# Kernel tuning notes

Hardware: AMD Instinct MI355X
Metric: run time of the kernel (lower is better)

Reference implementation:

```python
import jax, jax.numpy as jnp
import numpy as np

T = 2048          # num tokens (prefill)
H = 4096          # hidden_size
NH = 32           # num query heads
NKV = 8           # num kv heads (GQA)
HD = H // NH      # head_dim = 128
BASE = 1000000.0  # rope_theta
NEG = -1e30


def _rope(x, positions):
    # NeoX-style rotary embedding (vLLM default). x: [T, nh, HD]
    half = HD // 2
    inv_freq = 1.0 / (BASE ** (jnp.arange(half, dtype=jnp.float32) / half))
    freqs = positions.astype(jnp.float32)[:, None] * inv_freq  # [T, half]
    cos = jnp.concatenate([jnp.cos(freqs), jnp.cos(freqs)], -1)[:, None, :]
    sin = jnp.concatenate([jnp.sin(freqs), jnp.sin(freqs)], -1)[:, None, :]
    rot = jnp.concatenate([-x[..., half:], x[..., :half]], -1)
    return x * cos + rot * sin


def setup_inputs() -> dict:
    key = jax.random.key(0)
    k1, k2, k3 = jax.random.split(key, 3)
    hidden_states = jax.random.normal(k1, (T, H), jnp.float32)
    wqkv = jax.random.normal(k2, (H, (NH + 2 * NKV) * HD), jnp.float32) * 0.02
    wo = jax.random.normal(k3, (NH * HD, H), jnp.float32) * 0.02
    positions = jnp.arange(T, dtype=jnp.int32)
    return {"positions": positions, "hidden_states": hidden_states,
            "wqkv": wqkv, "wo": wo}


def reference(positions, hidden_states, wqkv, wo):
    # fused QKV projection
    qkv = hidden_states @ wqkv                      # [T, (NH+2*NKV)*HD]
    q, k, v = jnp.split(qkv, [NH * HD, NH * HD + NKV * HD], axis=-1)
    q = q.reshape(T, NH, HD)
    k = k.reshape(T, NKV, HD)
    v = v.reshape(T, NKV, HD)
    # inline RoPE on q, k
    q = _rope(q, positions)
    k = _rope(k, positions)
    # GQA: expand kv heads to query heads
    rep = NH // NKV
    k = jnp.repeat(k, rep, axis=1)                  # [T, NH, HD]
    v = jnp.repeat(v, rep, axis=1)
    # causal scaled dot-product attention (prefill path of PagedAttention)
    scores = jnp.einsum('qhd,khd->hqk', q, k) * (HD ** -0.5)  # [NH, T, T]
    causal = positions[:, None] >= positions[None, :]          # [T, T]
    scores = jnp.where(causal[None, :, :], scores, NEG)
    probs = jax.nn.softmax(scores, axis=-1)
    attn = jnp.einsum('hqk,khd->qhd', probs, v).reshape(T, NH * HD)
    return attn @ wo
```

## Files before the change

kernel.cpp:

```cpp
#include <hip/hip_runtime.h>
#include <hip/hip_bf16.h>

typedef __attribute__((ext_vector_type(8))) short bf16x8;
typedef __attribute__((ext_vector_type(4))) float f32x4;
typedef unsigned short u16;

#define T_TOK 2048
#define HID 4096
#define NH 32
#define NKV 8
#define HD 128
#define QKVN 6144
#define KOFF 4096
#define VOFF 5120
#define ATTN_SCALE 0.08838834764831845f

static __device__ __forceinline__ float bf2f(u16 x) {
    union { float f; unsigned u; } v; v.u = ((unsigned)x) << 16; return v.f;
}
static __device__ __forceinline__ u16 f2bf(float f) {
    union { float f; unsigned u; } v; v.f = f;
    unsigned u = v.u;
    unsigned r = (u + 0x7fff + ((u >> 16) & 1)) >> 16;
    return (u16)r;
}

static __device__ __forceinline__ void gload16(const u16* g, u16* l) {
    __builtin_amdgcn_global_load_lds((const __attribute__((address_space(1))) void*)g,
                                     (__attribute__((address_space(3))) void*)l, 16, 0, 0);
}

#define VMC(n) asm volatile("s_waitcnt vmcnt(%0)" :: "i"(n) : "memory")
#define LGKM0() asm volatile("s_waitcnt lgkmcnt(0)" ::: "memory")
#define BAR() __builtin_amdgcn_s_barrier()
#define SCHB() __builtin_amdgcn_sched_barrier(0)

__global__ __launch_bounds__(256) void convk(const float* __restrict__ in, u16* __restrict__ out) {
    int i = blockIdx.x * 256 + threadIdx.x;
    float4 v = ((const float4*)in)[i];
    ushort4 o;
    o.x = f2bf(v.x); o.y = f2bf(v.y); o.z = f2bf(v.z); o.w = f2bf(v.w);
    ((ushort4*)out)[i] = o;
}

__global__ __launch_bounds__(256) void transpk(const float* __restrict__ in, u16* __restrict__ out,
                                               int R, int C) {
    __shared__ float tile[64][65];
    int c0 = blockIdx.x * 64, r0 = blockIdx.y * 64;
    int tid = threadIdx.x;
#pragma unroll
    for (int it = 0; it < 4; ++it) {
        int ci = it * 256 + tid;
        int r = ci >> 4, c4 = (ci & 15) * 4;
        float4 v = *(const float4*)&in[(size_t)(r0 + r) * C + c0 + c4];
        tile[r][c4 + 0] = v.x; tile[r][c4 + 1] = v.y; tile[r][c4 + 2] = v.z; tile[r][c4 + 3] = v.w;
    }
    __syncthreads();
#pragma unroll
    for (int it = 0; it < 4; ++it) {
        int ci = it * 256 + tid;
        int c = ci >> 4, rq = (ci & 15) * 4;
        ushort4 o;
        o.x = f2bf(tile[rq + 0][c]); o.y = f2bf(tile[rq + 1][c]);
        o.z = f2bf(tile[rq + 2][c]); o.w = f2bf(tile[rq + 3][c]);
        *(ushort4*)&out[(size_t)(c0 + c) * R + r0 + rq] = o;
    }
}

template <int BN, int OUTF32>
__global__ __launch_bounds__(512) void gemm4p(const u16* __restrict__ A, const u16* __restrict__ Bt,
                                              void* __restrict__ Cout, int M, int N, int K) {
    constexpr int NF = BN / 64;
    constexpr int LB = BN / 128;
    constexpr int DBUF = (128 + BN) * 64;
    constexpr int BHALF = (BN / 2) * 64;
    __shared__ __attribute__((aligned(16))) u16 lds[2 * DBUF];

    int bid = blockIdx.x;
    int m0 = (bid & 15) * 128, n0 = (bid >> 4) * BN;
    int tid = threadIdx.x, lane = tid & 63, wid = tid >> 6;
    int wm = wid >> 2, wn = wid & 3;
    int l15 = lane & 15, g4 = lane >> 4;
    int sw = l15 & 7;
    int srow = tid >> 3;
    int sslot8 = (((tid & 7) ^ ((tid >> 3) & 7))) * 8;
    int brow0 = (wn & 1) * (BN / 4);
    int NK = K / 64;

    auto STAGE_A = [&](int kt, int h) {
        gload16(&A[(size_t)(m0 + h * 64 + srow) * K + kt * 64 + sslot8],
                &lds[(kt & 1) * DBUF + h * 4096 + wid * 512]);
    };
    auto STAGE_B = [&](int kt, int bh) {
#pragma unroll
        for (int it = 0; it < LB; ++it)
            gload16(&Bt[(size_t)(n0 + bh * (BN / 2) + it * 64 + srow) * K + kt * 64 + sslot8],
                    &lds[(kt & 1) * DBUF + 8192 + bh * BHALF + it * 4096 + wid * 512]);
    };

    f32x4 acc[4][NF];
#pragma unroll
    for (int i = 0; i < 4; ++i)
#pragma unroll
        for (int j = 0; j < NF; ++j) acc[i][j] = (f32x4){0.f, 0.f, 0.f, 0.f};

    STAGE_A(0, 0); STAGE_A(0, 1); STAGE_B(0, 0); STAGE_B(0, 1);
    STAGE_A(1, 0); STAGE_A(1, 1); STAGE_B(1, 0); STAGE_B(1, 1);
    VMC(2 + 2 * LB);
    BAR(); SCHB();

    for (int g = 0; g < NK; ++g) {
        const u16* dd = &lds[(g & 1) * DBUF];
        const u16* aw = dd + wm * 4096;
        const u16* bw = dd + 8192 + (wn >> 1) * BHALF;
        bool mid = (g > 0) && (g + 1 < NK);
        bf16x8 bfr[NF], af0, af1;

#pragma unroll
        for (int nf = 0; nf < NF; ++nf)
            bfr[nf] = *(const bf16x8*)&bw[(brow0 + nf * 16 + l15) * 64 + ((g4 ^ sw) * 8)];
        af0 = *(const bf16x8*)&aw[(0 * 16 + l15) * 64 + ((g4 ^ sw) * 8)];
        af1 = *(const bf16x8*)&aw[(1 * 16 + l15) * 64 + ((g4 ^ sw) * 8)];
        if (mid) STAGE_A(g + 1, 0);
        BAR(); LGKM0();
        __builtin_amdgcn_s_setprio(1);
#pragma unroll
        for (int nf = 0; nf < NF; ++nf) {
            acc[0][nf] = __builtin_amdgcn_mfma_f32_16x16x32_bf16(af0, bfr[nf], acc[0][nf], 0, 0, 0);
            acc[1][nf] = __builtin_amdgcn_mfma_f32_16x16x32_bf16(af1, bfr[nf], acc[1][nf], 0, 0, 0);
        }
        __builtin_amdgcn_s_setprio(0);
        BAR();

        af0 = *(const bf16x8*)&aw[(2 * 16 + l15) * 64 + ((g4 ^ sw) * 8)];
        af1 = *(const bf16x8*)&aw[(3 * 16 + l15) * 64 + ((g4 ^ sw) * 8)];
        if (mid) STAGE_B(g + 1, 1);
        BAR(); LGKM0();
        __builtin_amdgcn_s_setprio(1);
#pragma unroll
        for (int nf = 0; nf < NF; ++nf) {
            acc[2][nf] = __builtin_amdgcn_mfma_f32_16x16x32_bf16(af0, bfr[nf], acc[2][nf], 0, 0, 0);
            acc[3][nf] = __builtin_amdgcn_mfma_f32_16x16x32_bf16(af1, bfr[nf], acc[3][nf], 0, 0, 0);
        }
        __builtin_amdgcn_s_setprio(0);
        BAR();

#pragma unroll
        for (int nf = 0; nf < NF; ++nf)
            bfr[nf] = *(const bf16x8*)&bw[(brow0 + nf * 16 + l15) * 64 + (((4 + g4) ^ sw) * 8)];
        af0 = *(const bf16x8*)&aw[(0 * 16 + l15) * 64 + (((4 + g4) ^ sw) * 8)];
        af1 = *(const bf16x8*)&aw[(1 * 16 + l15) * 64 + (((4 + g4) ^ sw) * 8)];
        if (mid) STAGE_A(g + 1, 1);
        BAR(); LGKM0();
        __builtin_amdgcn_s_setprio(1);
#pragma unroll
        for (int nf = 0; nf < NF; ++nf) {
            acc[0][nf] = __builtin_amdgcn_mfma_f32_16x16x32_bf16(af0, bfr[nf], acc[0][nf], 0, 0, 0);
            acc[1][nf] = __builtin_amdgcn_mfma_f32_16x16x32_bf16(af1, bfr[nf], acc[1][nf], 0, 0, 0);
        }
        __builtin_amdgcn_s_setprio(0);
        BAR();

        af0 = *(const bf16x8*)&aw[(2 * 16 + l15) * 64 + (((4 + g4) ^ sw) * 8)];
        af1 = *(const bf16x8*)&aw[(3 * 16 + l15) * 64 + (((4 + g4) ^ sw) * 8)];
        if (g + 2 < NK) STAGE_B(g + 2, 0);
        BAR(); LGKM0();
        __builtin_amdgcn_s_setprio(1);
#pragma unroll
        for (int nf = 0; nf < NF; ++nf) {
            acc[2][nf] = __builtin_amdgcn_mfma_f32_16x16x32_bf16(af0, bfr[nf], acc[2][nf], 0, 0, 0);
            acc[3][nf] = __builtin_amdgcn_mfma_f32_16x16x32_bf16(af1, bfr[nf], acc[3][nf], 0, 0, 0);
        }
        __builtin_amdgcn_s_setprio(0);
        if (g <= NK - 3)      VMC(LB);
        else if (g == NK - 2) VMC(0);
        BAR(); SCHB();
    }

#pragma unroll
    for (int mf = 0; mf < 4; ++mf)
#pragma unroll
        for (int nf = 0; nf < NF; ++nf)
#pragma unroll
            for (int i = 0; i < 4; ++i) {
                int row = m0 + wm * 64 + mf * 16 + g4 * 4 + i;
                int col = n0 + wn * (BN / 4) + nf * 16 + l15;
                float v = acc[mf][nf][i];
                if (OUTF32) ((float*)Cout)[(size_t)row * N + col] = v;
                else        ((u16*)Cout)[(size_t)row * N + col] = f2bf(v);
            }
}

__global__ __launch_bounds__(256) void ropek(u16* __restrict__ qkvb, const int* __restrict__ positions) {
    __shared__ float cs_[64], sn_[64];
    int t = blockIdx.x;
    float pos = (float)positions[t];
    if (threadIdx.x < 64) {
        int d = threadIdx.x;
        float inv = exp2f(-(float)d * (19.931568569324174f / 64.0f));
        float fr = pos * inv;
        cs_[d] = cosf(fr);
        sn_[d] = sinf(fr);
    }
    __syncthreads();
#pragma unroll
    for (int it = 0; it < 10; ++it) {
        int ci = it * 256 + threadIdx.x;
        int hh = ci >> 6, d = ci & 63;
        int base = (hh < NH) ? hh * HD : KOFF + (hh - NH) * HD;
        size_t off = (size_t)t * QKVN + base + d;
        float x1 = bf2f(qkvb[off]);
        float x2 = bf2f(qkvb[off + 64]);
        float s = sn_[d], c = cs_[d];
        float y1 = x1 * c - x2 * s;
        float y2 = x2 * c + x1 * s;
        if (hh < NH) { y1 *= ATTN_SCALE; y2 *= ATTN_SCALE; }
        qkvb[off]      = f2bf(y1);
        qkvb[off + 64] = f2bf(y2);
    }
}

__global__ __launch_bounds__(256) void vtranspk(const u16* __restrict__ qkvb, u16* __restrict__ vT) {
    __shared__ __attribute__((aligned(16))) u16 tile[64][136];
    int kvh = blockIdx.x, t0 = blockIdx.y * 64;
    int tid = threadIdx.x;
#pragma unroll
    for (int it = 0; it < 4; ++it) {
        int ci = it * 256 + tid;
        int r = ci >> 4, c8 = (ci & 15) * 8;
        *(bf16x8*)&tile[r][c8] = *(const bf16x8*)&qkvb[(size_t)(t0 + r) * QKVN + VOFF + kvh * HD + c8];
    }
    __syncthreads();
#pragma unroll
    for (int it = 0; it < 4; ++it) {
        int ci = it * 256 + tid;
        int d = ci >> 3, tc = (ci & 7) * 8;
        union { bf16x8 v; u16 u[8]; } o;
#pragma unroll
        for (int e = 0; e < 8; ++e) o.u[e] = tile[tc + e][d];
        *(bf16x8*)&vT[((size_t)kvh * HD + d) * T_TOK + t0 + tc] = o.v;
    }
}

__global__ __launch_bounds__(512) void attnk(const u16* __restrict__ qkvb, const u16* __restrict__ vT,
                                             u16* __restrict__ attnb) {
    __shared__ __attribute__((aligned(16))) u16 kt_[64 * 136];
    __shared__ __attribute__((aligned(16))) u16 vt_[128 * 72];
    __shared__ __attribute__((aligned(16))) u16 pl_[8 * 16 * 72];
    int h = blockIdx.x, qt = 15 - blockIdx.y;
    int kvh = h >> 2;
    int q0 = qt * 128;
    int tid = threadIdx.x, lane = tid & 63, wid = tid >> 6;
    int l15 = lane & 15, g = lane >> 4;

    const u16* kbase = qkvb + KOFF + (size_t)kvh * HD;
    const u16* vbase = vT + (size_t)kvh * HD * T_TOK;

    bf16x8 qf[4];
    int qrow = q0 + wid * 16 + l15;
#pragma unroll
    for (int ks = 0; ks < 4; ++ks)
        qf[ks] = *(const bf16x8*)&qkvb[(size_t)qrow * QKVN + h * HD + ks * 32 + g * 8];

    f32x4 o[8];
#pragma unroll
    for (int df = 0; df < 8; ++df) o[df] = (f32x4){0.f, 0.f, 0.f, 0.f};
    float m_run[4], l_run[4];
#pragma unroll
    for (int i = 0; i < 4; ++i) { m_run[i] = -3.0e38f; l_run[i] = 0.f; }

    int NT = 2 * qt + 2;

    bf16x8 kreg[2], vreg[2];
#pragma unroll
    for (int it = 0; it < 2; ++it) {
        int gi = it * 512 + tid;
        kreg[it] = *(const bf16x8*)&kbase[(size_t)(gi >> 4) * QKVN + (gi & 15) * 8];
        vreg[it] = *(const bf16x8*)&vbase[(size_t)(gi >> 3) * T_TOK + (gi & 7) * 8];
    }
#pragma unroll
    for (int it = 0; it < 2; ++it) {
        int gi = it * 512 + tid;
        *(bf16x8*)&kt_[(gi >> 4) * 136 + (gi & 15) * 8] = kreg[it];
        *(bf16x8*)&vt_[(gi >> 3) * 72 + (gi & 7) * 8] = vreg[it];
    }
#pragma unroll
    for (int it = 0; it < 2; ++it) {
        int gi = it * 512 + tid;
        kreg[it] = *(const bf16x8*)&kbase[(size_t)(64 + (gi >> 4)) * QKVN + (gi & 15) * 8];
        vreg[it] = *(const bf16x8*)&vbase[(size_t)(gi >> 3) * T_TOK + 64 + (gi & 7) * 8];
    }
    __syncthreads();

    for (int kt2 = 0; kt2 < NT; ++kt2) {
        int kvb = kt2 * 64;
        bool active = (kvb <= q0 + wid * 16 + 15);
        bool diag   = (kvb + 63 > q0 + wid * 16);

        if (active) {
            f32x4 s[4];
#pragma unroll
            for (int nf = 0; nf < 4; ++nf) s[nf] = (f32x4){0.f, 0.f, 0.f, 0.f};
            __builtin_amdgcn_s_setprio(1);
#pragma unroll
            for (int ks = 0; ks < 4; ++ks) {
#pragma unroll
                for (int nf = 0; nf < 4; ++nf) {
                    bf16x8 bfr = *(const bf16x8*)&kt_[(nf * 16 + l15) * 136 + ks * 32 + g * 8];
                    s[nf] = __builtin_amdgcn_mfma_f32_16x16x32_bf16(qf[ks], bfr, s[nf], 0, 0, 0);
                }
            }
            __builtin_amdgcn_s_setprio(0);

            float mrow[4];
#pragma unroll
            for (int i = 0; i < 4; ++i) {
                int qr = q0 + wid * 16 + g * 4 + i;
                float mx = -3.0e38f;
#pragma unroll
                for (int nf = 0; nf < 4; ++nf) {
                    float v = s[nf][i];
                    if (diag) {
                        int kvc = kvb + nf * 16 + l15;
                        v = (kvc <= qr) ? v : -1.0e30f;
                        s[nf][i] = v;
                    }
                    mx = fmaxf(mx, v);
                }
                mrow[i] = mx;
            }
#pragma unroll
            for (int dd = 1; dd < 16; dd <<= 1)
#pragma unroll
                for (int i = 0; i < 4; ++i) mrow[i] = fmaxf(mrow[i], __shfl_xor(mrow[i], dd));

            int ok = 1;
#pragma unroll
            for (int i = 0; i < 4; ++i) ok &= (mrow[i] <= m_run[i] + 8.0f) ? 1 : 0;
            if (!__all(ok)) {
                float alpha[4];
#pragma unroll
                for (int i = 0; i < 4; ++i) {
                    float mnew = fmaxf(m_run[i], mrow[i]);
                    alpha[i] = __expf(m_run[i] - mnew);
                    m_run[i] = mnew;
                    l_run[i] *= alpha[i];
                }
#pragma unroll
                for (int df = 0; df < 8; ++df)
#pragma unroll
                    for (int i = 0; i < 4; ++i) o[df][i] *= alpha[i];
            }

            float rsum[4] = {0.f, 0.f, 0.f, 0.f};
#pragma unroll
            for (int nf = 0; nf < 4; ++nf)
#pragma unroll
                for (int i = 0; i < 4; ++i) {
                    float p = __expf(s[nf][i] - m_run[i]);
                    rsum[i] += p;
                    pl_[wid * 1152 + (g * 4 + i) * 72 + nf * 16 + l15] = f2bf(p);
                }
#pragma unroll
            for (int dd = 1; dd < 16; dd <<= 1)
#pragma unroll
                for (int i = 0; i < 4; ++i) rsum[i] += __shfl_xor(rsum[i], dd);
#pragma unroll
            for (int i = 0; i < 4; ++i) l_run[i] += rsum[i];

            __builtin_amdgcn_s_setprio(1);
#pragma unroll
            for (int ks2 = 0; ks2 < 2; ++ks2) {
                bf16x8 af = *(const bf16x8*)&pl_[wid * 1152 + l15 * 72 + ks2 * 32 + g * 8];
#pragma unroll
                for (int df = 0; df < 8; ++df) {
                    bf16x8 bfr = *(const bf16x8*)&vt_[(df * 16 + l15) * 72 + ks2 * 32 + g * 8];
                    o[df] = __builtin_amdgcn_mfma_f32_16x16x32_bf16(af, bfr, o[df], 0, 0, 0);
                }
            }
            __builtin_amdgcn_s_setprio(0);
        }

        if (kt2 < NT - 1) {
            __syncthreads();
#pragma unroll
            for (int it = 0; it < 2; ++it) {
                int gi = it * 512 + tid;
                *(bf16x8*)&kt_[(gi >> 4) * 136 + (gi & 15) * 8] = kreg[it];
                *(bf16x8*)&vt_[(gi >> 3) * 72 + (gi & 7) * 8] = vreg[it];
            }
            int ktl = (kt2 + 2 < NT) ? kt2 + 2 : NT - 1;
#pragma unroll
            for (int it = 0; it < 2; ++it) {
                int gi = it * 512 + tid;
                kreg[it] = *(const bf16x8*)&kbase[(size_t)(ktl * 64 + (gi >> 4)) * QKVN + (gi & 15) * 8];
                vreg[it] = *(const bf16x8*)&vbase[(size_t)(gi >> 3) * T_TOK + ktl * 64 + (gi & 7) * 8];
            }
            __syncthreads();
        }
    }

#pragma unroll
    for (int df = 0; df < 8; ++df)
#pragma unroll
        for (int i = 0; i < 4; ++i) {
            int qr = q0 + wid * 16 + g * 4 + i;
            int col = h * HD + df * 16 + l15;
            attnb[(size_t)qr * (NH * HD) + col] = f2bf(o[df][i] / l_run[i]);
        }
}

extern "C" void kernel_launch(void* const* d_in, const int* in_sizes, int n_in,
                              void* d_out, int out_size, void* d_ws, size_t ws_size,
                              hipStream_t stream) {
    const int*   positions = (const int*)d_in[0];
    const float* hs        = (const float*)d_in[1];
    const float* wqkv      = (const float*)d_in[2];
    const float* wo        = (const float*)d_in[3];
    float* out = (float*)d_out;

    char* ws = (char*)d_ws;
    u16* hsb   = (u16*)(ws);
    u16* wqkvT = (u16*)(ws + 16777216);
    u16* woT   = (u16*)(ws + 16777216 + 50331648);
    u16* qkvb  = (u16*)(ws + 16777216 + 50331648 + 33554432);
    u16* vT    = (u16*)(ws + 16777216 + 50331648 + 33554432 + 25165824);
    u16* attnb = hsb;

    convk<<<8192, 256, 0, stream>>>(hs, hsb);
    transpk<<<dim3(96, 64), 256, 0, stream>>>(wqkv, wqkvT, HID, QKVN);
    transpk<<<dim3(64, 64), 256, 0, stream>>>(wo, woT, HID, HID);

    gemm4p<384, 0><<<dim3(256), 512, 0, stream>>>(hsb, wqkvT, qkvb, T_TOK, QKVN, HID);

    ropek<<<T_TOK, 256, 0, stream>>>(qkvb, positions);

    vtranspk<<<dim3(NKV, 32), 256, 0, stream>>>(qkvb, vT);

    attnk<<<dim3(NH, 16), 512, 0, stream>>>(qkvb, vT, attnb);

    gemm4p<256, 1><<<dim3(256), 512, 0, stream>>>(attnb, woT, out, T_TOK, HID, HID);
}
```

Baseline: 334.0 us.

## Add 256x256-tile QKV GEMM and shrink attention LDS row padding

Adds a new GEMM kernel for the QKV projection that computes a 256x256 output tile per 512-thread block. It splits each K=64 step into four MFMA phases and interleaves the async global-to-LDS staging of the next tile between them. The goal is more operand reuse per LDS load and less global traffic than the previous 128x384 tiling. The trade-off is a 192-block grid, which leaves some compute units idle, and a large double-buffered LDS footprint. Separately, the attention kernel's LDS row paddings shrink from 136/72 to 132/68 elements to change the bank mapping, which leaves the 16-byte vector LDS accesses no longer 16-byte aligned.

```diff
diff --git a/kernel.cpp b/kernel.cpp
--- a/kernel.cpp
+++ b/kernel.cpp
@@ -65,6 +65,120 @@
         o.z = f2bf(tile[rq + 2][c]); o.w = f2bf(tile[rq + 3][c]);
         *(ushort4*)&out[(size_t)(c0 + c) * R + r0 + rq] = o;
     }
+}
+
+__global__ __launch_bounds__(512, 2) void gemm256(const u16* __restrict__ A, const u16* __restrict__ Bt,
+                                                  u16* __restrict__ Cout, int M, int N, int K) {
+    constexpr int DBUF = 512 * 64;
+    __shared__ __attribute__((aligned(16))) u16 lds[2 * DBUF];
+
+    int bid = blockIdx.x;
+    int m0 = (bid & 7) * 256, n0 = (bid >> 3) * 256;
+    int tid = threadIdx.x, lane = tid & 63, wid = tid >> 6;
+    int wm = wid >> 2, wn = wid & 3;
+    int l15 = lane & 15, g4 = lane >> 4;
+    int sw = l15 & 7;
+    int srow8 = tid >> 3;
+    int sslot8 = ((tid & 7) ^ (srow8 & 7)) * 8;
+    int NK = K / 64;
+
+    auto STAGE = [&](int kt, int c) {
+        u16* dst = &lds[(kt & 1) * DBUF + c * 4096 + wid * 512];
+        const u16* src = (c < 4)
+            ? &A[(size_t)(m0 + c * 64 + srow8) * K + kt * 64 + sslot8]
+            : &Bt[(size_t)(n0 + (c - 4) * 64 + srow8) * K + kt * 64 + sslot8];
+        gload16(src, dst);
+    };
+
+    f32x4 acc[8][4];
+#pragma unroll
+    for (int i = 0; i < 8; ++i)
+#pragma unroll
+        for (int j = 0; j < 4; ++j) acc[i][j] = (f32x4){0.f, 0.f, 0.f, 0.f};
+
+#pragma unroll
+    for (int c = 0; c < 8; ++c) STAGE(0, c);
+    VMC(0);
+    BAR(); SCHB();
+
+    for (int g = 0; g < NK; ++g) {
+        const u16* ab = &lds[(g & 1) * DBUF];
+        const u16* bb = ab + 16384;
+        bool st = (g + 1 < NK);
+        bf16x8 af[8], af2[8], b0, b1;
+
+#pragma unroll
+        for (int mi = 0; mi < 8; ++mi)
+            af[mi] = *(const bf16x8*)&ab[(wm * 128 + mi * 16 + l15) * 64 + ((g4 ^ sw) * 8)];
+        b0 = *(const bf16x8*)&bb[(wn * 64 + 0 * 16 + l15) * 64 + ((g4 ^ sw) * 8)];
+        b1 = *(const bf16x8*)&bb[(wn * 64 + 1 * 16 + l15) * 64 + ((g4 ^ sw) * 8)];
+        if (st) { STAGE(g + 1, 0); STAGE(g + 1, 1); STAGE(g + 1, 4); }
+        BAR(); LGKM0();
+        __builtin_amdgcn_s_setprio(1);
+#pragma unroll
+        for (int mi = 0; mi < 8; ++mi) {
+            acc[mi][0] = __builtin_amdgcn_mfma_f32_16x16x32_bf16(af[mi], b0, acc[mi][0], 0, 0, 0);
+            acc[mi][1] = __builtin_amdgcn_mfma_f32_16x16x32_bf16(af[mi], b1, acc[mi][1], 0, 0, 0);
+        }
+        __builtin_amdgcn_s_setprio(0);
+        BAR();
+
+        b0 = *(const bf16x8*)&bb[(wn * 64 + 2 * 16 + l15) * 64 + ((g4 ^ sw) * 8)];
+        b1 = *(const bf16x8*)&bb[(wn * 64 + 3 * 16 + l15) * 64 + ((g4 ^ sw) * 8)];
+#pragma unroll
+        for (int mi = 0; mi < 4; ++mi)
+            af2[mi] = *(const bf16x8*)&ab[(wm * 128 + mi * 16 + l15) * 64 + (((4 + g4) ^ sw) * 8)];
+        if (st) { STAGE(g + 1, 2); STAGE(g + 1, 3); STAGE(g + 1, 5); }
+        BAR(); LGKM0();
+        __builtin_amdgcn_s_setprio(1);
+#pragma unroll
+        for (int mi = 0; mi < 8; ++mi) {
+            acc[mi][2] = __builtin_amdgcn_mfma_f32_16x16x32_bf16(af[mi], b0, acc[mi][2], 0, 0, 0);
+            acc[mi][3] = __builtin_amdgcn_mfma_f32_16x16x32_bf16(af[mi], b1, acc[mi][3], 0, 0, 0);
+        }
+        __builtin_amdgcn_s_setprio(0);
+        BAR();
+
+#pragma unroll
+        for (int mi = 4; mi < 8; ++mi)
+            af2[mi] = *(const bf16x8*)&ab[(wm * 128 + mi * 16 + l15) * 64 + (((4 + g4) ^ sw) * 8)];
+        b0 = *(const bf16x8*)&bb[(wn * 64 + 0 * 16 + l15) * 64 + (((4 + g4) ^ sw) * 8)];
+        b1 = *(const bf16x8*)&bb[(wn * 64 + 1 * 16 + l15) * 64 + (((4 + g4) ^ sw) * 8)];
+        if (st) { STAGE(g + 1, 6); STAGE(g + 1, 7); }
+        BAR(); LGKM0();
+        __builtin_amdgcn_s_setprio(1);
+#pragma unroll
+        for (int mi = 0; mi < 8; ++mi) {
+            acc[mi][0] = __builtin_amdgcn_mfma_f32_16x16x32_bf16(af2[mi], b0, acc[mi][0], 0, 0, 0);
+            acc[mi][1] = __builtin_amdgcn_mfma_f32_16x16x32_bf16(af2[mi], b1, acc[mi][1], 0, 0, 0);
+        }
+        __builtin_amdgcn_s_setprio(0);
+        BAR();
+
+        b0 = *(const bf16x8*)&bb[(wn * 64 + 2 * 16 + l15) * 64 + (((4 + g4) ^ sw) * 8)];
+        b1 = *(const bf16x8*)&bb[(wn * 64 + 3 * 16 + l15) * 64 + (((4 + g4) ^ sw) * 8)];
+        BAR(); LGKM0();
+        __builtin_amdgcn_s_setprio(1);
+#pragma unroll
+        for (int mi = 0; mi < 8; ++mi) {
+            acc[mi][2] = __builtin_amdgcn_mfma_f32_16x16x32_bf16(af2[mi], b0, acc[mi][2], 0, 0, 0);
+            acc[mi][3] = __builtin_amdgcn_mfma_f32_16x16x32_bf16(af2[mi], b1, acc[mi][3], 0, 0, 0);
+        }
+        __builtin_amdgcn_s_setprio(0);
+        if (st) VMC(0);
+        BAR(); SCHB();
+    }
+
+#pragma unroll
+    for (int mi = 0; mi < 8; ++mi)
+#pragma unroll
+        for (int nj = 0; nj < 4; ++nj)
+#pragma unroll
+            for (int i = 0; i < 4; ++i) {
+                int row = m0 + wm * 128 + mi * 16 + g4 * 4 + i;
+                int col = n0 + wn * 64 + nj * 16 + l15;
+                Cout[(size_t)row * N + col] = f2bf(acc[mi][nj][i]);
+            }
 }
 
 template <int BN, int OUTF32>
@@ -244,9 +358,9 @@
 
 __global__ __launch_bounds__(512) void attnk(const u16* __restrict__ qkvb, const u16* __restrict__ vT,
                                              u16* __restrict__ attnb) {
-    __shared__ __attribute__((aligned(16))) u16 kt_[64 * 136];
-    __shared__ __attribute__((aligned(16))) u16 vt_[128 * 72];
-    __shared__ __attribute__((aligned(16))) u16 pl_[8 * 16 * 72];
+    __shared__ __attribute__((aligned(16))) u16 kt_[64 * 132];
+    __shared__ __attribute__((aligned(16))) u16 vt_[128 * 68];
+    __shared__ __attribute__((aligned(16))) u16 pl_[8 * 16 * 68];
     int h = blockIdx.x, qt = 15 - blockIdx.y;
     int kvh = h >> 2;
     int q0 = qt * 128;
@@ -281,8 +395,8 @@
 #pragma unroll
     for (int it = 0; it < 2; ++it) {
         int gi = it * 512 + tid;
-        *(bf16x8*)&kt_[(gi >> 4) * 136 + (gi & 15) * 8] = kreg[it];
-        *(bf16x8*)&vt_[(gi >> 3) * 72 + (gi & 7) * 8] = vreg[it];
+        *(bf16x8*)&kt_[(gi >> 4) * 132 + (gi & 15) * 8] = kreg[it];
+        *(bf16x8*)&vt_[(gi >> 3) * 68 + (gi & 7) * 8] = vreg[it];
     }
 #pragma unroll
     for (int it = 0; it < 2; ++it) {
@@ -306,7 +420,7 @@
             for (int ks = 0; ks < 4; ++ks) {
 #pragma unroll
                 for (int nf = 0; nf < 4; ++nf) {
-                    bf16x8 bfr = *(const bf16x8*)&kt_[(nf * 16 + l15) * 136 + ks * 32 + g * 8];
+                    bf16x8 bfr = *(const bf16x8*)&kt_[(nf * 16 + l15) * 132 + ks * 32 + g * 8];
                     s[nf] = __builtin_amdgcn_mfma_f32_16x16x32_bf16(qf[ks], bfr, s[nf], 0, 0, 0);
                 }
             }
@@ -359,7 +473,7 @@
                 for (int i = 0; i < 4; ++i) {
                     float p = __expf(s[nf][i] - m_run[i]);
                     rsum[i] += p;
-                    pl_[wid * 1152 + (g * 4 + i) * 72 + nf * 16 + l15] = f2bf(p);
+                    pl_[wid * 1088 + (g * 4 + i) * 68 + nf * 16 + l15] = f2bf(p);
                 }
 #pragma unroll
             for (int dd = 1; dd < 16; dd <<= 1)
@@ -371,10 +485,10 @@
             __builtin_amdgcn_s_setprio(1);
 #pragma unroll
             for (int ks2 = 0; ks2 < 2; ++ks2) {
-                bf16x8 af = *(const bf16x8*)&pl_[wid * 1152 + l15 * 72 + ks2 * 32 + g * 8];
+                bf16x8 af = *(const bf16x8*)&pl_[wid * 1088 + l15 * 68 + ks2 * 32 + g * 8];
 #pragma unroll
                 for (int df = 0; df < 8; ++df) {
-                    bf16x8 bfr = *(const bf16x8*)&vt_[(df * 16 + l15) * 72 + ks2 * 32 + g * 8];
+                    bf16x8 bfr = *(const bf16x8*)&vt_[(df * 16 + l15) * 68 + ks2 * 32 + g * 8];
                     o[df] = __builtin_amdgcn_mfma_f32_16x16x32_bf16(af, bfr, o[df], 0, 0, 0);
                 }
             }
@@ -386,8 +500,8 @@
 #pragma unroll
             for (int it = 0; it < 2; ++it) {
                 int gi = it * 512 + tid;
-                *(bf16x8*)&kt_[(gi >> 4) * 136 + (gi & 15) * 8] = kreg[it];
-                *(bf16x8*)&vt_[(gi >> 3) * 72 + (gi & 7) * 8] = vreg[it];
+                *(bf16x8*)&kt_[(gi >> 4) * 132 + (gi & 15) * 8] = kreg[it];
+                *(bf16x8*)&vt_[(gi >> 3) * 68 + (gi & 7) * 8] = vreg[it];
             }
             int ktl = (kt2 + 2 < NT) ? kt2 + 2 : NT - 1;
 #pragma unroll
@@ -431,7 +545,7 @@
     transpk<<<dim3(96, 64), 256, 0, stream>>>(wqkv, wqkvT, HID, QKVN);
     transpk<<<dim3(64, 64), 256, 0, stream>>>(wo, woT, HID, HID);
 
-    gemm4p<384, 0><<<dim3(256), 512, 0, stream>>>(hsb, wqkvT, qkvb, T_TOK, QKVN, HID);
+    gemm256<<<dim3(192), 512, 0, stream>>>(hsb, wqkvT, qkvb, T_TOK, QKVN, HID);
 
     ropek<<<T_TOK, 256, 0, stream>>>(qkvb, positions);
 
```

After: 346.4 us. 3.7% more time.

## Add 4-stage 256xBN QKV GEMM and widen attention waves to 32 rows

Applied to the files above, without the earlier changes.

Introduces gemm8p, a 256-row tile GEMM with a 4-deep LDS ring of BK=32 slices, swizzled LDS reads, and async global-to-LDS staging split across the two MFMA halves. The QKV projection now uses it with BN=192. Separately, the attention kernel drops to 256 threads, with each wave handling 32 query rows (two MFMA row blocks) that share the K and V fragment loads. LDS padding also shrinks. This raises per-wave register pressure and halves the threads per block, aiming for more reuse and less LDS traffic per MFMA.

```diff
diff --git a/kernel.cpp b/kernel.cpp
--- a/kernel.cpp
+++ b/kernel.cpp
@@ -65,6 +65,114 @@
         o.z = f2bf(tile[rq + 2][c]); o.w = f2bf(tile[rq + 3][c]);
         *(ushort4*)&out[(size_t)(c0 + c) * R + r0 + rq] = o;
     }
+}
+
+template <int BN, int OUTF32>
+__global__ __launch_bounds__(512) void gemm8p(const u16* __restrict__ A, const u16* __restrict__ Bt,
+                                              void* __restrict__ Cout, int M, int N, int K) {
+    constexpr int BM = 256, BK = 32;
+    constexpr int WN = BN / 4;
+    constexpr int NF = WN / 16;
+    constexpr int BCH = BN / 16;
+    constexpr int CA = 2 + (BCH + 7) / 8;
+    constexpr int CB = 2 + BCH / 8;
+    constexpr int ABUF = BM * BK;
+    constexpr int BBUF = BN * BK;
+    constexpr int BUFSZ = ABUF + BBUF;
+
+    __shared__ __attribute__((aligned(16))) u16 lds[4 * BUFSZ];
+
+    int bid = blockIdx.x;
+    int m0 = (bid & 7) * BM, n0 = (bid >> 3) * BN;
+    int tid = threadIdx.x, lane = tid & 63, wid = tid >> 6;
+    int wm = wid >> 2, wn = wid & 3;
+    int l15 = lane & 15, g4 = lane >> 4;
+    int srow = lane >> 2;
+    int sslot = (lane & 3) ^ ((lane >> 3) & 3);
+    int swz = (g4 ^ ((l15 >> 1) & 3)) * 8;
+    int NK = K / BK;
+    bool shortw = (CA != CB) && (wid >= 4);
+
+    auto STAGE = [&](int kt, int c) {
+        u16* base = &lds[(kt & 3) * BUFSZ];
+        size_t kcol = (size_t)kt * BK + sslot * 8;
+        if (c < 2) {
+            int ch = wid * 2 + c;
+            gload16(&A[(size_t)(m0 + ch * 16 + srow) * K + kcol], base + ch * 512);
+        } else {
+            int ch = (c - 2) * 8 + wid;
+            if (ch < BCH)
+                gload16(&Bt[(size_t)(n0 + ch * 16 + srow) * K + kcol], base + ABUF + ch * 512);
+        }
+    };
+
+    f32x4 acc[8][NF];
+#pragma unroll
+    for (int i = 0; i < 8; ++i)
+#pragma unroll
+        for (int j = 0; j < NF; ++j) acc[i][j] = (f32x4){0.f, 0.f, 0.f, 0.f};
+
+    for (int t = 0; t < 3; ++t)
+        for (int c = 0; c < CA; ++c) STAGE(t, c);
+    if (shortw) VMC(2 * CB); else VMC(2 * CA);
+    BAR(); SCHB();
+
+    for (int g = 0; g < NK; ++g) {
+        const u16* ab = &lds[(g & 3) * BUFSZ];
+        const u16* bb = ab + ABUF;
+
+        bf16x8 bfr[NF], af[4];
+#pragma unroll
+        for (int j = 0; j < NF; ++j)
+            bfr[j] = *(const bf16x8*)&bb[(wn * WN + j * 16 + l15) * BK + swz];
+#pragma unroll
+        for (int i = 0; i < 4; ++i)
+            af[i] = *(const bf16x8*)&ab[(wm * 128 + i * 16 + l15) * BK + swz];
+        if (g + 3 < NK) {
+            STAGE(g + 3, 0); STAGE(g + 3, 1);
+        }
+        __builtin_amdgcn_s_setprio(1);
+#pragma unroll
+        for (int i = 0; i < 4; ++i)
+#pragma unroll
+            for (int j = 0; j < NF; ++j)
+                acc[i][j] = __builtin_amdgcn_mfma_f32_16x16x32_bf16(af[i], bfr[j], acc[i][j], 0, 0, 0);
+        __builtin_amdgcn_s_setprio(0);
+
+        bf16x8 af2[4];
+#pragma unroll
+        for (int i = 0; i < 4; ++i)
+            af2[i] = *(const bf16x8*)&ab[(wm * 128 + (4 + i) * 16 + l15) * BK + swz];
+        if (g + 3 < NK) {
+#pragma unroll
+            for (int c = 2; c < CA; ++c) STAGE(g + 3, c);
+        }
+        __builtin_amdgcn_s_setprio(1);
+#pragma unroll
+        for (int i = 0; i < 4; ++i)
+#pragma unroll
+            for (int j = 0; j < NF; ++j)
+                acc[4 + i][j] = __builtin_amdgcn_mfma_f32_16x16x32_bf16(af2[i], bfr[j], acc[4 + i][j], 0, 0, 0);
+        __builtin_amdgcn_s_setprio(0);
+
+        if (g < NK - 3)       { if (shortw) VMC(2 * CB); else VMC(2 * CA); }
+        else if (g == NK - 3) { if (shortw) VMC(CB);     else VMC(CA); }
+        else if (g == NK - 2) VMC(0);
+        BAR(); SCHB();
+    }
+
+#pragma unroll
+    for (int mi = 0; mi < 8; ++mi)
+#pragma unroll
+        for (int j = 0; j < NF; ++j)
+#pragma unroll
+            for (int i = 0; i < 4; ++i) {
+                int row = m0 + wm * 128 + mi * 16 + g4 * 4 + i;
+                int col = n0 + wn * WN + j * 16 + l15;
+                float v = acc[mi][j][i];
+                if (OUTF32) ((float*)Cout)[(size_t)row * N + col] = v;
+                else        ((u16*)Cout)[(size_t)row * N + col] = f2bf(v);
+            }
 }
 
 template <int BN, int OUTF32>
@@ -242,11 +350,11 @@
     }
 }
 
-__global__ __launch_bounds__(512) void attnk(const u16* __restrict__ qkvb, const u16* __restrict__ vT,
+__global__ __launch_bounds__(256) void attnk(const u16* __restrict__ qkvb, const u16* __restrict__ vT,
                                              u16* __restrict__ attnb) {
-    __shared__ __attribute__((aligned(16))) u16 kt_[64 * 136];
-    __shared__ __attribute__((aligned(16))) u16 vt_[128 * 72];
-    __shared__ __attribute__((aligned(16))) u16 pl_[8 * 16 * 72];
+    __shared__ __attribute__((aligned(16))) u16 kt_[64 * 132];
+    __shared__ __attribute__((aligned(16))) u16 vt_[128 * 68];
+    __shared__ __attribute__((aligned(16))) u16 pl_[4 * 32 * 68];
     int h = blockIdx.x, qt = 15 - blockIdx.y;
     int kvh = h >> 2;
     int q0 = qt * 128;
@@ -256,37 +364,44 @@
     const u16* kbase = qkvb + KOFF + (size_t)kvh * HD;
     const u16* vbase = vT + (size_t)kvh * HD * T_TOK;
 
-    bf16x8 qf[4];
-    int qrow = q0 + wid * 16 + l15;
-#pragma unroll
-    for (int ks = 0; ks < 4; ++ks)
-        qf[ks] = *(const bf16x8*)&qkvb[(size_t)qrow * QKVN + h * HD + ks * 32 + g * 8];
-
-    f32x4 o[8];
-#pragma unroll
-    for (int df = 0; df < 8; ++df) o[df] = (f32x4){0.f, 0.f, 0.f, 0.f};
-    float m_run[4], l_run[4];
-#pragma unroll
-    for (int i = 0; i < 4; ++i) { m_run[i] = -3.0e38f; l_run[i] = 0.f; }
+    bf16x8 qf[2][4];
+#pragma unroll
+    for (int mi = 0; mi < 2; ++mi) {
+        int qrow = q0 + wid * 32 + mi * 16 + l15;
+#pragma unroll
+        for (int ks = 0; ks < 4; ++ks)
+            qf[mi][ks] = *(const bf16x8*)&qkvb[(size_t)qrow * QKVN + h * HD + ks * 32 + g * 8];
+    }
+
+    f32x4 o[2][8];
+#pragma unroll
+    for (int mi = 0; mi < 2; ++mi)
+#pragma unroll
+        for (int df = 0; df < 8; ++df) o[mi][df] = (f32x4){0.f, 0.f, 0.f, 0.f};
+    float m_run[2][4], l_run[2][4];
+#pragma unroll
+    for (int mi = 0; mi < 2; ++mi)
+#pragma unroll
+        for (int i = 0; i < 4; ++i) { m_run[mi][i] = -3.0e38f; l_run[mi][i] = 0.f; }
 
     int NT = 2 * qt + 2;
 
-    bf16x8 kreg[2], vreg[2];
-#pragma unroll
-    for (int it = 0; it < 2; ++it) {
-        int gi = it * 512 + tid;
+    bf16x8 kreg[4], vreg[4];
+#pragma unroll
+    for (int it = 0; it < 4; ++it) {
+        int gi = it * 256 + tid;
         kreg[it] = *(const bf16x8*)&kbase[(size_t)(gi >> 4) * QKVN + (gi & 15) * 8];
         vreg[it] = *(const bf16x8*)&vbase[(size_t)(gi >> 3) * T_TOK + (gi & 7) * 8];
     }
 #pragma unroll
-    for (int it = 0; it < 2; ++it) {
-        int gi = it * 512 + tid;
-        *(bf16x8*)&kt_[(gi >> 4) * 136 + (gi & 15) * 8] = kreg[it];
-        *(bf16x8*)&vt_[(gi >> 3) * 72 + (gi & 7) * 8] = vreg[it];
-    }
-#pragma unroll
-    for (int it = 0; it < 2; ++it) {
-        int gi = it * 512 + tid;
+    for (int it = 0; it < 4; ++it) {
+        int gi = it * 256 + tid;
+        *(bf16x8*)&kt_[(gi >> 4) * 132 + (gi & 15) * 8] = kreg[it];
+        *(bf16x8*)&vt_[(gi >> 3) * 68 + (gi & 7) * 8] = vreg[it];
+    }
+#pragma unroll
+    for (int it = 0; it < 4; ++it) {
+        int gi = it * 256 + tid;
         kreg[it] = *(const bf16x8*)&kbase[(size_t)(64 + (gi >> 4)) * QKVN + (gi & 15) * 8];
         vreg[it] = *(const bf16x8*)&vbase[(size_t)(gi >> 3) * T_TOK + 64 + (gi & 7) * 8];
     }
@@ -294,88 +409,109 @@
 
     for (int kt2 = 0; kt2 < NT; ++kt2) {
         int kvb = kt2 * 64;
-        bool active = (kvb <= q0 + wid * 16 + 15);
-        bool diag   = (kvb + 63 > q0 + wid * 16);
+        bool active = (kvb <= q0 + wid * 32 + 31);
+        bool diag   = (kvb + 63 > q0 + wid * 32);
 
         if (active) {
-            f32x4 s[4];
-#pragma unroll
-            for (int nf = 0; nf < 4; ++nf) s[nf] = (f32x4){0.f, 0.f, 0.f, 0.f};
+            f32x4 s[2][4];
+#pragma unroll
+            for (int mi = 0; mi < 2; ++mi)
+#pragma unroll
+                for (int nf = 0; nf < 4; ++nf) s[mi][nf] = (f32x4){0.f, 0.f, 0.f, 0.f};
             __builtin_amdgcn_s_setprio(1);
 #pragma unroll
             for (int ks = 0; ks < 4; ++ks) {
 #pragma unroll
                 for (int nf = 0; nf < 4; ++nf) {
-                    bf16x8 bfr = *(const bf16x8*)&kt_[(nf * 16 + l15) * 136 + ks * 32 + g * 8];
-                    s[nf] = __builtin_amdgcn_mfma_f32_16x16x32_bf16(qf[ks], bfr, s[nf], 0, 0, 0);
+                    bf16x8 bfr = *(const bf16x8*)&kt_[(nf * 16 + l15) * 132 + ks * 32 + g * 8];
+#pragma unroll
+                    for (int mi = 0; mi < 2; ++mi)
+                        s[mi][nf] = __builtin_amdgcn_mfma_f32_16x16x32_bf16(qf[mi][ks], bfr, s[mi][nf], 0, 0, 0);
                 }
             }
             __builtin_amdgcn_s_setprio(0);
 
-            float mrow[4];
-#pragma unroll
-            for (int i = 0; i < 4; ++i) {
-                int qr = q0 + wid * 16 + g * 4 + i;
-                float mx = -3.0e38f;
-#pragma unroll
-                for (int nf = 0; nf < 4; ++nf) {
-                    float v = s[nf][i];
-                    if (diag) {
-                        int kvc = kvb + nf * 16 + l15;
-                        v = (kvc <= qr) ? v : -1.0e30f;
-                        s[nf][i] = v;
+            float mrow[2][4];
+#pragma unroll
+            for (int mi = 0; mi < 2; ++mi)
+#pragma unroll
+                for (int i = 0; i < 4; ++i) {
+                    int qr = q0 + wid * 32 + mi * 16 + g * 4 + i;
+                    float mx = -3.0e38f;
+#pragma unroll
+                    for (int nf = 0; nf < 4; ++nf) {
+                        float v = s[mi][nf][i];
+                        if (diag) {
+                            int kvc = kvb + nf * 16 + l15;
+                            v = (kvc <= qr) ? v : -1.0e30f;
+                            s[mi][nf][i] = v;
+                        }
+                        mx = fmaxf(mx, v);
                     }
-                    mx = fmaxf(mx, v);
+                    mrow[mi][i] = mx;
                 }
-                mrow[i] = mx;
-            }
 #pragma unroll
             for (int dd = 1; dd < 16; dd <<= 1)
 #pragma unroll
-                for (int i = 0; i < 4; ++i) mrow[i] = fmaxf(mrow[i], __shfl_xor(mrow[i], dd));
+                for (int mi = 0; mi < 2; ++mi)
+#pragma unroll
+                    for (int i = 0; i < 4; ++i) mrow[mi][i] = fmaxf(mrow[mi][i], __shfl_xor(mrow[mi][i], dd));
 
             int ok = 1;
 #pragma unroll
-            for (int i = 0; i < 4; ++i) ok &= (mrow[i] <= m_run[i] + 8.0f) ? 1 : 0;
+            for (int mi = 0; mi < 2; ++mi)
+#pragma unroll
+                for (int i = 0; i < 4; ++i) ok &= (mrow[mi][i] <= m_run[mi][i] + 8.0f) ? 1 : 0;
             if (!__all(ok)) {
-                float alpha[4];
-#pragma unroll
-                for (int i = 0; i < 4; ++i) {
-                    float mnew = fmaxf(m_run[i], mrow[i]);
-                    alpha[i] = __expf(m_run[i] - mnew);
-                    m_run[i] = mnew;
-                    l_run[i] *= alpha[i];
+#pragma unroll
+                for (int mi = 0; mi < 2; ++mi) {
+                    float alpha[4];
+#pragma unroll
+                    for (int i = 0; i < 4; ++i) {
+                        float mnew = fmaxf(m_run[mi][i], mrow[mi][i]);
+                        alpha[i] = __expf(m_run[mi][i] - mnew);
+                        m_run[mi][i] = mnew;
+                        l_run[mi][i] *= alpha[i];
+                    }
+#pragma unroll
+                    for (int df = 0; df < 8; ++df)
+#pragma unroll
+                        for (int i = 0; i < 4; ++i) o[mi][df][i] *= alpha[i];
                 }
-#pragma unroll
-                for (int df = 0; df < 8; ++df)
-#pragma unroll
-                    for (int i = 0; i < 4; ++i) o[df][i] *= alpha[i];
-            }
-
-            float rsum[4] = {0.f, 0.f, 0.f, 0.f};
-#pragma unroll
-            for (int nf = 0; nf < 4; ++nf)
-#pragma unroll
-                for (int i = 0; i < 4; ++i) {
-                    float p = __expf(s[nf][i] - m_run[i]);
-                    rsum[i] += p;
-                    pl_[wid * 1152 + (g * 4 + i) * 72 + nf * 16 + l15] = f2bf(p);
-                }
+            }
+
+            float rsum[2][4] = {{0.f, 0.f, 0.f, 0.f}, {0.f, 0.f, 0.f, 0.f}};
+#pragma unroll
+            for (int mi = 0; mi < 2; ++mi)
+#pragma unroll
+                for (int nf = 0; nf < 4; ++nf)
+#pragma unroll
+                    for (int i = 0; i < 4; ++i) {
+                        float p = __expf(s[mi][nf][i] - m_run[mi][i]);
+                        rsum[mi][i] += p;
+                        pl_[wid * 2176 + (mi * 16 + g * 4 + i) * 68 + nf * 16 + l15] = f2bf(p);
+                    }
 #pragma unroll
             for (int dd = 1; dd < 16; dd <<= 1)
 #pragma unroll
-                for (int i = 0; i < 4; ++i) rsum[i] += __shfl_xor(rsum[i], dd);
-#pragma unroll
-            for (int i = 0; i < 4; ++i) l_run[i] += rsum[i];
+                for (int mi = 0; mi < 2; ++mi)
+#pragma unroll
+                    for (int i = 0; i < 4; ++i) rsum[mi][i] += __shfl_xor(rsum[mi][i], dd);
+#pragma unroll
+            for (int mi = 0; mi < 2; ++mi)
+#pragma unroll
+                for (int i = 0; i < 4; ++i) l_run[mi][i] += rsum[mi][i];
 
             __builtin_amdgcn_s_setprio(1);
 #pragma unroll
             for (int ks2 = 0; ks2 < 2; ++ks2) {
-                bf16x8 af = *(const bf16x8*)&pl_[wid * 1152 + l15 * 72 + ks2 * 32 + g * 8];
+                bf16x8 af0 = *(const bf16x8*)&pl_[wid * 2176 + (0 * 16 + l15) * 68 + ks2 * 32 + g * 8];
+                bf16x8 af1 = *(const bf16x8*)&pl_[wid * 2176 + (1 * 16 + l15) * 68 + ks2 * 32 + g * 8];
 #pragma unroll
                 for (int df = 0; df < 8; ++df) {
-                    bf16x8 bfr = *(const bf16x8*)&vt_[(df * 16 + l15) * 72 + ks2 * 32 + g * 8];
-                    o[df] = __builtin_amdgcn_mfma_f32_16x16x32_bf16(af, bfr, o[df], 0, 0, 0);
+                    bf16x8 bfr = *(const bf16x8*)&vt_[(df * 16 + l15) * 68 + ks2 * 32 + g * 8];
+                    o[0][df] = __builtin_amdgcn_mfma_f32_16x16x32_bf16(af0, bfr, o[0][df], 0, 0, 0);
+                    o[1][df] = __builtin_amdgcn_mfma_f32_16x16x32_bf16(af1, bfr, o[1][df], 0, 0, 0);
                 }
             }
             __builtin_amdgcn_s_setprio(0);
@@ -384,15 +520,15 @@
         if (kt2 < NT - 1) {
             __syncthreads();
 #pragma unroll
-            for (int it = 0; it < 2; ++it) {
-                int gi = it * 512 + tid;
-                *(bf16x8*)&kt_[(gi >> 4) * 136 + (gi & 15) * 8] = kreg[it];
-                *(bf16x8*)&vt_[(gi >> 3) * 72 + (gi & 7) * 8] = vreg[it];
+            for (int it = 0; it < 4; ++it) {
+                int gi = it * 256 + tid;
+                *(bf16x8*)&kt_[(gi >> 4) * 132 + (gi & 15) * 8] = kreg[it];
+                *(bf16x8*)&vt_[(gi >> 3) * 68 + (gi & 7) * 8] = vreg[it];
             }
             int ktl = (kt2 + 2 < NT) ? kt2 + 2 : NT - 1;
 #pragma unroll
-            for (int it = 0; it < 2; ++it) {
-                int gi = it * 512 + tid;
+            for (int it = 0; it < 4; ++it) {
+                int gi = it * 256 + tid;
                 kreg[it] = *(const bf16x8*)&kbase[(size_t)(ktl * 64 + (gi >> 4)) * QKVN + (gi & 15) * 8];
                 vreg[it] = *(const bf16x8*)&vbase[(size_t)(gi >> 3) * T_TOK + ktl * 64 + (gi & 7) * 8];
             }
@@ -401,13 +537,15 @@
     }
 
 #pragma unroll
-    for (int df = 0; df < 8; ++df)
-#pragma unroll
-        for (int i = 0; i < 4; ++i) {
-            int qr = q0 + wid * 16 + g * 4 + i;
-            int col = h * HD + df * 16 + l15;
-            attnb[(size_t)qr * (NH * HD) + col] = f2bf(o[df][i] / l_run[i]);
-        }
+    for (int mi = 0; mi < 2; ++mi)
+#pragma unroll
+        for (int df = 0; df < 8; ++df)
+#pragma unroll
+            for (int i = 0; i < 4; ++i) {
+                int qr = q0 + wid * 32 + mi * 16 + g * 4 + i;
+                int col = h * HD + df * 16 + l15;
+                attnb[(size_t)qr * (NH * HD) + col] = f2bf(o[mi][df][i] / l_run[mi][i]);
+            }
 }
 
 extern "C" void kernel_launch(void* const* d_in, const int* in_sizes, int n_in,
@@ -431,13 +569,13 @@
     transpk<<<dim3(96, 64), 256, 0, stream>>>(wqkv, wqkvT, HID, QKVN);
     transpk<<<dim3(64, 64), 256, 0, stream>>>(wo, woT, HID, HID);
 
-    gemm4p<384, 0><<<dim3(256), 512, 0, stream>>>(hsb, wqkvT, qkvb, T_TOK, QKVN, HID);
+    gemm8p<192, 0><<<dim3(256), 512, 0, stream>>>(hsb, wqkvT, qkvb, T_TOK, QKVN, HID);
 
     ropek<<<T_TOK, 256, 0, stream>>>(qkvb, positions);
 
     vtranspk<<<dim3(NKV, 32), 256, 0, stream>>>(qkvb, vT);
 
-    attnk<<<dim3(NH, 16), 512, 0, stream>>>(qkvb, vT, attnb);
+    attnk<<<dim3(NH, 16), 256, 0, stream>>>(qkvb, vT, attnb);
 
     gemm4p<256, 1><<<dim3(256), 512, 0, stream>>>(attnb, woT, out, T_TOK, HID, HID);
 }
```

Result: slower. 371.4 us (+11.2%).

## Add 256-row, 4-stage pipelined GEMM for QKV and retune attention LDS padding

Applied to the files above, without the earlier changes.

Adds a new GEMM kernel, gemm8p, with a 256xBN block tile, BK=32, and a 4-deep LDS ring buffer filled by direct global-to-LDS loads. Loads for future stages are interleaved between MFMA groups, and swizzled LDS reads aim to avoid bank conflicts. The QKV projection now uses this kernel with BN=192 instead of gemm4p<384>. Separately, the attention kernel's LDS row padding shrinks from 136/72 to 132/68 elements, which changes the bank-conflict pattern and LDS footprint. The deeper pipeline uses more LDS and adds more complex wait-count logic.

```diff
diff --git a/kernel.cpp b/kernel.cpp
--- a/kernel.cpp
+++ b/kernel.cpp
@@ -65,6 +65,112 @@
         o.z = f2bf(tile[rq + 2][c]); o.w = f2bf(tile[rq + 3][c]);
         *(ushort4*)&out[(size_t)(c0 + c) * R + r0 + rq] = o;
     }
+}
+
+template <int BN, int OUTF32>
+__global__ __launch_bounds__(512) void gemm8p(const u16* __restrict__ A, const u16* __restrict__ Bt,
+                                              void* __restrict__ Cout, int M, int N, int K) {
+    constexpr int BM = 256, BK = 32;
+    constexpr int WN = BN / 2;
+    constexpr int NF = WN / 16;
+    constexpr int BCH = BN / 16;
+    constexpr int CA = 2 + (BCH + 7) / 8;
+    constexpr int CB = 2 + BCH / 8;
+    constexpr int ABUF = BM * BK;
+    constexpr int BBUF = BN * BK;
+    constexpr int BUFSZ = ABUF + BBUF;
+
+    __shared__ __attribute__((aligned(16))) u16 lds[4 * BUFSZ];
+
+    int bid = blockIdx.x;
+    int m0 = (bid & 7) * BM, n0 = (bid >> 3) * BN;
+    int tid = threadIdx.x, lane = tid & 63, wid = tid >> 6;
+    int wm = wid >> 1, wn = wid & 1;
+    int l15 = lane & 15, g4 = lane >> 4;
+    int srow = lane >> 2;
+    int sslot = (lane & 3) ^ ((lane >> 3) & 3);
+    int swz = (g4 ^ ((l15 >> 1) & 3)) * 8;
+    int NK = K / BK;
+    bool shortw = (CA != CB) && (wid >= 4);
+
+    auto STAGE = [&](int kt, int c) {
+        u16* base = &lds[(kt & 3) * BUFSZ];
+        size_t kcol = (size_t)kt * BK + sslot * 8;
+        if (c < 2) {
+            int ch = wid * 2 + c;
+            gload16(&A[(size_t)(m0 + ch * 16 + srow) * K + kcol], base + ch * 512);
+        } else {
+            int ch = (c - 2) * 8 + wid;
+            if (ch < BCH)
+                gload16(&Bt[(size_t)(n0 + ch * 16 + srow) * K + kcol], base + ABUF + ch * 512);
+        }
+    };
+
+    f32x4 acc[4][NF];
+#pragma unroll
+    for (int i = 0; i < 4; ++i)
+#pragma unroll
+        for (int j = 0; j < NF; ++j) acc[i][j] = (f32x4){0.f, 0.f, 0.f, 0.f};
+
+    for (int t = 0; t < 3; ++t)
+        for (int c = 0; c < CA; ++c) STAGE(t, c);
+    if (shortw) VMC(2 * CB); else VMC(2 * CA);
+    BAR(); SCHB();
+
+    for (int g = 0; g < NK; ++g) {
+        const u16* ab = &lds[(g & 3) * BUFSZ];
+        const u16* bb = ab + ABUF;
+
+        bf16x8 bfr[NF], af0, af1;
+#pragma unroll
+        for (int j = 0; j < NF; ++j)
+            bfr[j] = *(const bf16x8*)&bb[(wn * WN + j * 16 + l15) * BK + swz];
+        af0 = *(const bf16x8*)&ab[(wm * 64 + 0 * 16 + l15) * BK + swz];
+        af1 = *(const bf16x8*)&ab[(wm * 64 + 1 * 16 + l15) * BK + swz];
+        if (g + 3 < NK) {
+            STAGE(g + 3, 0); STAGE(g + 3, 1);
+        }
+        __builtin_amdgcn_s_setprio(1);
+#pragma unroll
+        for (int j = 0; j < NF; ++j) {
+            acc[0][j] = __builtin_amdgcn_mfma_f32_16x16x32_bf16(af0, bfr[j], acc[0][j], 0, 0, 0);
+            acc[1][j] = __builtin_amdgcn_mfma_f32_16x16x32_bf16(af1, bfr[j], acc[1][j], 0, 0, 0);
+        }
+        __builtin_amdgcn_s_setprio(0);
+
+        bf16x8 af2, af3;
+        af2 = *(const bf16x8*)&ab[(wm * 64 + 2 * 16 + l15) * BK + swz];
+        af3 = *(const bf16x8*)&ab[(wm * 64 + 3 * 16 + l15) * BK + swz];
+        if (g + 3 < NK) {
+#pragma unroll
+            for (int c = 2; c < CA; ++c) STAGE(g + 3, c);
+        }
+        __builtin_amdgcn_s_setprio(1);
+#pragma unroll
+        for (int j = 0; j < NF; ++j) {
+            acc[2][j] = __builtin_amdgcn_mfma_f32_16x16x32_bf16(af2, bfr[j], acc[2][j], 0, 0, 0);
+            acc[3][j] = __builtin_amdgcn_mfma_f32_16x16x32_bf16(af3, bfr[j], acc[3][j], 0, 0, 0);
+        }
+        __builtin_amdgcn_s_setprio(0);
+
+        if (g < NK - 3)       { if (shortw) VMC(2 * CB); else VMC(2 * CA); }
+        else if (g == NK - 3) { if (shortw) VMC(CB);     else VMC(CA); }
+        else if (g == NK - 2) VMC(0);
+        BAR(); SCHB();
+    }
+
+#pragma unroll
+    for (int mi = 0; mi < 4; ++mi)
+#pragma unroll
+        for (int j = 0; j < NF; ++j)
+#pragma unroll
+            for (int i = 0; i < 4; ++i) {
+                int row = m0 + wm * 64 + mi * 16 + g4 * 4 + i;
+                int col = n0 + wn * WN + j * 16 + l15;
+                float v = acc[mi][j][i];
+                if (OUTF32) ((float*)Cout)[(size_t)row * N + col] = v;
+                else        ((u16*)Cout)[(size_t)row * N + col] = f2bf(v);
+            }
 }
 
 template <int BN, int OUTF32>
@@ -244,9 +350,9 @@
 
 __global__ __launch_bounds__(512) void attnk(const u16* __restrict__ qkvb, const u16* __restrict__ vT,
                                              u16* __restrict__ attnb) {
-    __shared__ __attribute__((aligned(16))) u16 kt_[64 * 136];
-    __shared__ __attribute__((aligned(16))) u16 vt_[128 * 72];
-    __shared__ __attribute__((aligned(16))) u16 pl_[8 * 16 * 72];
+    __shared__ __attribute__((aligned(16))) u16 kt_[64 * 132];
+    __shared__ __attribute__((aligned(16))) u16 vt_[128 * 68];
+    __shared__ __attribute__((aligned(16))) u16 pl_[8 * 16 * 68];
     int h = blockIdx.x, qt = 15 - blockIdx.y;
     int kvh = h >> 2;
     int q0 = qt * 128;
@@ -281,8 +387,8 @@
 #pragma unroll
     for (int it = 0; it < 2; ++it) {
         int gi = it * 512 + tid;
-        *(bf16x8*)&kt_[(gi >> 4) * 136 + (gi & 15) * 8] = kreg[it];
-        *(bf16x8*)&vt_[(gi >> 3) * 72 + (gi & 7) * 8] = vreg[it];
+        *(bf16x8*)&kt_[(gi >> 4) * 132 + (gi & 15) * 8] = kreg[it];
+        *(bf16x8*)&vt_[(gi >> 3) * 68 + (gi & 7) * 8] = vreg[it];
     }
 #pragma unroll
     for (int it = 0; it < 2; ++it) {
@@ -306,7 +412,7 @@
             for (int ks = 0; ks < 4; ++ks) {
 #pragma unroll
                 for (int nf = 0; nf < 4; ++nf) {
-                    bf16x8 bfr = *(const bf16x8*)&kt_[(nf * 16 + l15) * 136 + ks * 32 + g * 8];
+                    bf16x8 bfr = *(const bf16x8*)&kt_[(nf * 16 + l15) * 132 + ks * 32 + g * 8];
                     s[nf] = __builtin_amdgcn_mfma_f32_16x16x32_bf16(qf[ks], bfr, s[nf], 0, 0, 0);
                 }
             }
@@ -359,7 +465,7 @@
                 for (int i = 0; i < 4; ++i) {
                     float p = __expf(s[nf][i] - m_run[i]);
                     rsum[i] += p;
-                    pl_[wid * 1152 + (g * 4 + i) * 72 + nf * 16 + l15] = f2bf(p);
+                    pl_[wid * 1088 + (g * 4 + i) * 68 + nf * 16 + l15] = f2bf(p);
                 }
 #pragma unroll
             for (int dd = 1; dd < 16; dd <<= 1)
@@ -371,10 +477,10 @@
             __builtin_amdgcn_s_setprio(1);
 #pragma unroll
             for (int ks2 = 0; ks2 < 2; ++ks2) {
-                bf16x8 af = *(const bf16x8*)&pl_[wid * 1152 + l15 * 72 + ks2 * 32 + g * 8];
+                bf16x8 af = *(const bf16x8*)&pl_[wid * 1088 + l15 * 68 + ks2 * 32 + g * 8];
 #pragma unroll
                 for (int df = 0; df < 8; ++df) {
-                    bf16x8 bfr = *(const bf16x8*)&vt_[(df * 16 + l15) * 72 + ks2 * 32 + g * 8];
+                    bf16x8 bfr = *(const bf16x8*)&vt_[(df * 16 + l15) * 68 + ks2 * 32 + g * 8];
                     o[df] = __builtin_amdgcn_mfma_f32_16x16x32_bf16(af, bfr, o[df], 0, 0, 0);
                 }
             }
@@ -386,8 +492,8 @@
 #pragma unroll
             for (int it = 0; it < 2; ++it) {
                 int gi = it * 512 + tid;
-                *(bf16x8*)&kt_[(gi >> 4) * 136 + (gi & 15) * 8] = kreg[it];
-                *(bf16x8*)&vt_[(gi >> 3) * 72 + (gi & 7) * 8] = vreg[it];
+                *(bf16x8*)&kt_[(gi >> 4) * 132 + (gi & 15) * 8] = kreg[it];
+                *(bf16x8*)&vt_[(gi >> 3) * 68 + (gi & 7) * 8] = vreg[it];
             }
             int ktl = (kt2 + 2 < NT) ? kt2 + 2 : NT - 1;
 #pragma unroll
@@ -431,7 +537,7 @@
     transpk<<<dim3(96, 64), 256, 0, stream>>>(wqkv, wqkvT, HID, QKVN);
     transpk<<<dim3(64, 64), 256, 0, stream>>>(wo, woT, HID, HID);
 
-    gemm4p<384, 0><<<dim3(256), 512, 0, stream>>>(hsb, wqkvT, qkvb, T_TOK, QKVN, HID);
+    gemm8p<192, 0><<<dim3(256), 512, 0, stream>>>(hsb, wqkvT, qkvb, T_TOK, QKVN, HID);
 
     ropek<<<T_TOK, 256, 0, stream>>>(qkvb, positions);
 
```

New measurement: 339.6 us. No clear change (+1.7%).
